# Kernel optimization log

Hardware: AMD Instinct MI355X
Metric: run time of the kernel (lower is better)

Reference implementation:

```python
import jax, jax.numpy as jnp
import numpy as np

N = 100000        # nodes
E_HALF = 800000   # random edges before symmetrization
HID = 128         # hidden_dim
K = 4             # Chebyshev order
NEG = 0.01        # leaky_relu negative slope
BN_EPS = 1e-5
L2_EPS = 1e-12


def setup_inputs() -> dict:
    key = jax.random.key(0)
    ks = jax.random.split(key, 4)
    x = jax.random.normal(ks[0], (N, 3), dtype=jnp.float32)
    e = jax.random.randint(ks[1], (2, E_HALF), 0, N, dtype=jnp.int32)
    # symmetrize so the sym-normalized Laplacian is well defined
    edge_index = jnp.concatenate([e, e[::-1]], axis=1).astype(jnp.int64)

    def wcheb(k, fin, fout):
        return jax.random.normal(k, (K, fin, fout), dtype=jnp.float32) * np.float32(1.0 / np.sqrt(fin * K))

    wk = jax.random.split(ks[2], 5)
    return {
        "x": x, "edge_index": edge_index,
        "W1": wcheb(wk[0], 3, HID),   "b1": jnp.zeros((HID,), jnp.float32),
        "W2": wcheb(wk[1], HID, HID), "b2": jnp.zeros((HID,), jnp.float32),
        "W3": wcheb(wk[2], HID, HID), "b3": jnp.zeros((HID,), jnp.float32),
        "W4": wcheb(wk[3], HID, HID), "b4": jnp.zeros((HID,), jnp.float32),
        "g1": jnp.ones((HID,), jnp.float32), "be1": jnp.zeros((HID,), jnp.float32),
        "g2": jnp.ones((HID,), jnp.float32), "be2": jnp.zeros((HID,), jnp.float32),
        "g3": jnp.ones((HID,), jnp.float32), "be3": jnp.zeros((HID,), jnp.float32),
        "Wrep": jax.random.normal(wk[4], (HID, 3), dtype=jnp.float32) * np.float32(1.0 / np.sqrt(HID)),
        "brep": jnp.zeros((3,), jnp.float32),
    }


def _cheb(x, src, dst, norm, W, b):
    """PyG ChebConv (sym norm, lambda_max=2): out = sum_k T_k(L_hat) x @ W_k + b."""
    def prop(t):  # (L_hat t)_i = sum_{e: src->dst==i} norm_e * t[src_e]
        return jax.ops.segment_sum(t[src] * norm[:, None], dst, num_segments=N)
    Tx0 = x
    out = Tx0 @ W[0]
    Tx1 = prop(Tx0)
    out = out + Tx1 @ W[1]
    for k in range(2, W.shape[0]):
        Tx2 = 2.0 * prop(Tx1) - Tx0
        out = out + Tx2 @ W[k]
        Tx0, Tx1 = Tx1, Tx2
    return out + b


def _bn(x, g, b):  # BatchNorm1d, training mode (batch stats, biased var)
    mu = x.mean(axis=0)
    var = ((x - mu) ** 2).mean(axis=0)
    return (x - mu) * jax.lax.rsqrt(var + BN_EPS) * g + b


def _leaky(x):
    return jnp.where(x >= 0, x, NEG * x)


def reference(x, edge_index, W1, b1, W2, b2, W3, b3, W4, b4,
              g1, be1, g2, be2, g3, be3, Wrep, brep):
    src, dst = edge_index[0], edge_index[1]
    deg = jax.ops.segment_sum(jnp.ones(src.shape, jnp.float32), src, num_segments=N)
    dinv = jnp.where(deg > 0, jax.lax.rsqrt(jnp.maximum(deg, 1.0)), 0.0)
    # scaled Laplacian L_hat = -D^{-1/2} A D^{-1/2} (zero diagonal) for lambda_max=2
    norm = -(dinv[src] * dinv[dst])  # [E]

    h = _cheb(x.astype(jnp.float32), src, dst, norm, W1, b1)
    h = _bn(_leaky(h), g1, be1)
    h = _cheb(h, src, dst, norm, W2, b2)
    h = _bn(_leaky(h), g2, be2)
    h = _cheb(h, src, dst, norm, W3, b3)
    h = _bn(jnp.maximum(h, 0.0), g3, be3)
    h = _cheb(h, src, dst, norm, W4, b4)
    h = h / jnp.maximum(jnp.linalg.norm(h, axis=1, keepdims=True), L2_EPS)
    return h @ Wrep + brep  # [N, 3]
```

## Files before the change

kernel.cpp:

```cpp
#include <hip/hip_runtime.h>
#include <hip/hip_bf16.h>


#define HID 128
#define NEG 0.01f
#define BN_EPS 1e-5f
#define L2_EPS 1e-12f
#define CAP 64

typedef __attribute__((ext_vector_type(8))) short short8;
typedef __attribute__((ext_vector_type(4))) float floatx4;

__device__ __forceinline__ short f2bf(float f) {
    unsigned u = __float_as_uint(f);
    return (short)((u + 0x7fffu + ((u >> 16) & 1u)) >> 16);
}
__device__ __forceinline__ unsigned pack2bf(float x, float y) {
    return (unsigned)(unsigned short)f2bf(x) | ((unsigned)(unsigned short)f2bf(y) << 16);
}
__device__ __forceinline__ float bflo(unsigned u) { return __uint_as_float(u << 16); }
__device__ __forceinline__ float bfhi(unsigned u) { return __uint_as_float(u & 0xffff0000u); }
__device__ __forceinline__ float bf2f(unsigned short h) { return __uint_as_float((unsigned)h << 16); }

__device__ __forceinline__ float actf(float v, int act) {
    if (act == 0) return v >= 0.f ? v : NEG * v;
    if (act == 1) return v > 0.f ? v : 0.f;
    return v;
}


__global__ __launch_bounds__(256) void k_zero(int* __restrict__ arr, float* __restrict__ S,
                                              const float* __restrict__ x, float* __restrict__ xp, int N) {
    int i = blockIdx.x * 256 + threadIdx.x;
    if (i < N) {
        arr[(size_t)i * CAP] = 0;
        float4 v;
        v.x = x[(size_t)i * 3 + 0];
        v.y = x[(size_t)i * 3 + 1];
        v.z = x[(size_t)i * 3 + 2];
        v.w = 0.f;
        *(float4*)(xp + (size_t)i * 4) = v;
    }
    if (blockIdx.x == 0) {
        for (int k = threadIdx.x; k < 1024; k += 256) S[k] = 0.f;
    }
}

__global__ __launch_bounds__(256) void k_fillpad(const int* __restrict__ src, const int* __restrict__ dst,
                                                 int* __restrict__ arr, int E) {
    int e = blockIdx.x * 256 + threadIdx.x;
    if (e >= E) return;
    int d = dst[e];
    int pos = atomicAdd(&arr[(size_t)d * CAP], 1);
    if (pos < CAP - 1) arr[(size_t)d * CAP + 1 + pos] = src[e];
}

__global__ __launch_bounds__(256) void k_dinv(const int* __restrict__ arr, float* __restrict__ dinv,
                                              int* __restrict__ cnt, int N) {
    int i = blockIdx.x * 256 + threadIdx.x;
    if (i < N) {
        int d = arr[(size_t)i * CAP];
        dinv[i] = d > 0 ? rsqrtf((float)d) : 0.f;
        cnt[i] = d < CAP - 1 ? d : CAP - 1;
    }
}

__global__ __launch_bounds__(256) void k_norm(const int* __restrict__ arr, const int* __restrict__ cnt,
                                              const float* __restrict__ dinv, int2* __restrict__ edges,
                                              float* __restrict__ snorm, int N) {
    int node = blockIdx.x * 4 + (threadIdx.x >> 6);
    if (node >= N) return;
    node = __builtin_amdgcn_readfirstlane(node);
    int lane = threadIdx.x & 63;
    int deg = cnt[node];
    float dd = dinv[node];
    int s = (lane < deg) ? arr[(size_t)node * CAP + 1 + lane] : 0;
    float w = (lane < deg) ? -(dinv[s] * dd) : 0.f;
    if (lane < deg) {
        int2 rec;
        rec.x = s;
        rec.y = __float_as_int(w);
        edges[(size_t)node * CAP + lane] = rec;
    }
    float sw = w;
    #pragma unroll
    for (int d = 1; d < 64; d <<= 1) sw += __shfl_xor(sw, d);
    if (lane == 0) snorm[node] = sw;
}


__global__ __launch_bounds__(256) void k_prop3(const float* __restrict__ T, const float* __restrict__ prev,
                                               float* __restrict__ out, const int* __restrict__ cnt,
                                               const int2* __restrict__ edges,
                                               float a, float b, int N) {
    int i = blockIdx.x * 256 + threadIdx.x;
    if (i >= N) return;
    int deg = cnt[i];
    const int2* eb = edges + (size_t)i * CAP;
    float a0 = 0.f, a1 = 0.f, a2 = 0.f;
    int j = 0;
    for (; j + 4 <= deg; j += 4) {
        int2 r0 = eb[j + 0], r1 = eb[j + 1], r2 = eb[j + 2], r3 = eb[j + 3];
        float4 v0 = *(const float4*)(T + (size_t)r0.x * 4);
        float4 v1 = *(const float4*)(T + (size_t)r1.x * 4);
        float4 v2 = *(const float4*)(T + (size_t)r2.x * 4);
        float4 v3 = *(const float4*)(T + (size_t)r3.x * 4);
        float w0 = __int_as_float(r0.y), w1 = __int_as_float(r1.y);
        float w2 = __int_as_float(r2.y), w3 = __int_as_float(r3.y);
        a0 += w0 * v0.x + w1 * v1.x + w2 * v2.x + w3 * v3.x;
        a1 += w0 * v0.y + w1 * v1.y + w2 * v2.y + w3 * v3.y;
        a2 += w0 * v0.z + w1 * v1.z + w2 * v2.z + w3 * v3.z;
    }
    for (; j < deg; ++j) {
        int2 r = eb[j];
        float w = __int_as_float(r.y);
        float4 v = *(const float4*)(T + (size_t)r.x * 4);
        a0 += w * v.x;
        a1 += w * v.y;
        a2 += w * v.z;
    }
    float r0 = a * a0, r1 = a * a1, r2 = a * a2;
    if (prev) {
        const float* pp = prev + (size_t)i * 4;
        r0 += b * pp[0];
        r1 += b * pp[1];
        r2 += b * pp[2];
    }
    float4 o;
    o.x = r0; o.y = r1; o.z = r2; o.w = 0.f;
    *(float4*)(out + (size_t)i * 4) = o;
}

__global__ __launch_bounds__(256) void k_prop1(const unsigned* __restrict__ OUT,
                                               unsigned* __restrict__ T1, unsigned* __restrict__ T0,
                                               const int* __restrict__ cnt, const int2* __restrict__ edges,
                                               const float* __restrict__ snorm, const float* __restrict__ S,
                                               const float* __restrict__ g, const float* __restrict__ be,
                                               int act, float invN, int N) {
    int node = blockIdx.x * 4 + (threadIdx.x >> 6);
    if (node >= N) return;
    node = __builtin_amdgcn_readfirstlane(node);
    int lane = threadIdx.x & 63;
    int f0 = 2 * lane;
    float mu0 = S[f0] * invN, mu1 = S[f0 + 1] * invN;
    float v0 = S[f0 + 128] * invN - mu0 * mu0;
    float v1 = S[f0 + 129] * invN - mu1 * mu1;
    float a0 = g[f0] * rsqrtf(v0 + BN_EPS), a1 = g[f0 + 1] * rsqrtf(v1 + BN_EPS);
    float c0 = be[f0] - mu0 * a0, c1 = be[f0 + 1] - mu1 * a1;

    int deg = cnt[node];
    const int2* eb = edges + (size_t)node * CAP;
    float accx = 0.f, accy = 0.f;
    int j = 0;
    int nb = deg >> 3;
    if (nb > 0) {
        int2 recA[8]; unsigned tA[8];
        int2 recB[8]; unsigned tB[8];
        #pragma unroll
        for (int k = 0; k < 8; ++k) recA[k] = eb[k];
        #pragma unroll
        for (int k = 0; k < 8; ++k) tA[k] = OUT[(size_t)recA[k].x * 64 + lane];
        for (int bi = 1; bi < nb; ++bi) {
            const int2* ebb = eb + bi * 8;
            #pragma unroll
            for (int k = 0; k < 8; ++k) recB[k] = ebb[k];
            #pragma unroll
            for (int k = 0; k < 8; ++k) tB[k] = OUT[(size_t)recB[k].x * 64 + lane];
            #pragma unroll
            for (int k = 0; k < 8; ++k) {
                float w = __int_as_float(recA[k].y);
                accx += w * actf(bflo(tA[k]), act);
                accy += w * actf(bfhi(tA[k]), act);
            }
            #pragma unroll
            for (int k = 0; k < 8; ++k) { recA[k] = recB[k]; tA[k] = tB[k]; }
        }
        #pragma unroll
        for (int k = 0; k < 8; ++k) {
            float w = __int_as_float(recA[k].y);
            accx += w * actf(bflo(tA[k]), act);
            accy += w * actf(bfhi(tA[k]), act);
        }
        j = nb * 8;
    }
    for (; j < deg; ++j) {
        int2 r = eb[j];
        float w = __int_as_float(r.y);
        unsigned t0 = OUT[(size_t)r.x * 64 + lane];
        accx += w * actf(bflo(t0), act);
        accy += w * actf(bfhi(t0), act);
    }
    float si = snorm[node];
    __builtin_nontemporal_store(pack2bf(a0 * accx + si * c0, a1 * accy + si * c1),
                                &T1[(size_t)node * 64 + lane]);
    unsigned h = OUT[(size_t)node * 64 + lane];
    float t0lo = a0 * actf(bflo(h), act) + c0;
    float t0hi = a1 * actf(bfhi(h), act) + c1;
    __builtin_nontemporal_store(pack2bf(t0lo, t0hi), &T0[(size_t)node * 64 + lane]);
}

__global__ __launch_bounds__(256) void k_prop128(const unsigned* __restrict__ T, const unsigned* __restrict__ prev,
                                                 unsigned* __restrict__ out, const int* __restrict__ cnt,
                                                 const int2* __restrict__ edges,
                                                 float a, float b, int N) {
    int node = blockIdx.x * 4 + (threadIdx.x >> 6);
    if (node >= N) return;
    node = __builtin_amdgcn_readfirstlane(node);
    int lane = threadIdx.x & 63;
    int deg = cnt[node];
    const int2* eb = edges + (size_t)node * CAP;
    float accx = 0.f, accy = 0.f;
    int j = 0;
    int nb = deg >> 3;
    if (nb > 0) {
        int2 recA[8]; unsigned tA[8];
        int2 recB[8]; unsigned tB[8];
        #pragma unroll
        for (int k = 0; k < 8; ++k) recA[k] = eb[k];
        #pragma unroll
        for (int k = 0; k < 8; ++k) tA[k] = T[(size_t)recA[k].x * 64 + lane];
        for (int bi = 1; bi < nb; ++bi) {
            const int2* ebb = eb + bi * 8;
            #pragma unroll
            for (int k = 0; k < 8; ++k) recB[k] = ebb[k];
            #pragma unroll
            for (int k = 0; k < 8; ++k) tB[k] = T[(size_t)recB[k].x * 64 + lane];
            #pragma unroll
            for (int k = 0; k < 8; ++k) {
                float w = __int_as_float(recA[k].y);
                accx += w * bflo(tA[k]);
                accy += w * bfhi(tA[k]);
            }
            #pragma unroll
            for (int k = 0; k < 8; ++k) { recA[k] = recB[k]; tA[k] = tB[k]; }
        }
        #pragma unroll
        for (int k = 0; k < 8; ++k) {
            float w = __int_as_float(recA[k].y);
            accx += w * bflo(tA[k]);
            accy += w * bfhi(tA[k]);
        }
        j = nb * 8;
    }
    for (; j < deg; ++j) {
        int2 r = eb[j];
        float w = __int_as_float(r.y);
        unsigned t0 = T[(size_t)r.x * 64 + lane];
        accx += w * bflo(t0);
        accy += w * bfhi(t0);
    }
    float rx = a * accx, ry = a * accy;
    if (prev) {
        unsigned p = __builtin_nontemporal_load(&prev[(size_t)node * 64 + lane]);
        rx += b * bflo(p);
        ry += b * bfhi(p);
    }
    __builtin_nontemporal_store(pack2bf(rx, ry), &out[(size_t)node * 64 + lane]);
}


__global__ __launch_bounds__(256) void k_gemm1(const float* __restrict__ x, const float* __restrict__ t1,
                                               const float* __restrict__ t2, const float* __restrict__ t3,
                                               const float* __restrict__ W, const float* __restrict__ b,
                                               unsigned short* __restrict__ OUT, float* __restrict__ S,
                                               int npb, int N) {
    __shared__ float Wl[12 * 128];
    __shared__ float bl[128];
    __shared__ float sS[256];
    int tid = threadIdx.x;
    for (int i = tid; i < 1536; i += 256) Wl[i] = W[i];
    if (tid < 128) bl[tid] = b[tid];
    if (tid < 256) sS[tid] = 0.f;
    __syncthreads();
    int f = tid & 127;
    int base = blockIdx.x * npb;
    int end = base + npb < N ? base + npb : N;
    const float* rows[4] = {x, t1, t2, t3};
    float s1 = 0.f, s2 = 0.f;
    for (int node = base + (tid >> 7); node < end; node += 2) {
        float acc = bl[f];
        #pragma unroll
        for (int k = 0; k < 4; ++k) {
            float4 rv = *(const float4*)(rows[k] + (size_t)node * 4);
            acc += rv.x * Wl[(k * 3 + 0) * 128 + f];
            acc += rv.y * Wl[(k * 3 + 1) * 128 + f];
            acc += rv.z * Wl[(k * 3 + 2) * 128 + f];
        }
        unsigned short h = (unsigned short)f2bf(acc);
        OUT[(size_t)node * 128 + f] = h;
        float u = actf(bf2f(h), 0);
        s1 += u;
        s2 += u * u;
    }
    atomicAdd(&sS[f], s1);
    atomicAdd(&sS[f + 128], s2);
    __syncthreads();
    if (tid < 256) atomicAdd(&S[tid], sS[tid]);
}


__global__ __launch_bounds__(256) void k_packW(const float* __restrict__ WA, const float* __restrict__ WB,
                                               const float* __restrict__ WC, short* __restrict__ Wp) {
    int gid = blockIdx.x * 256 + threadIdx.x;
    int L = gid >> 16;
    int idx = gid & 65535;
    int j = idx & 7;
    int lane = (idx >> 3) & 63;
    int rest = idx >> 9;
    int nt = rest & 7;
    int ks = rest >> 3;
    int kk = ks * 32 + (lane >> 4) * 8 + j;
    int c = nt * 16 + (lane & 15);
    const float* W = (L == 0) ? WA : (L == 1) ? WB : WC;
    Wp[gid] = f2bf(W[(size_t)(kk >> 7) * 16384 + (kk & 127) * 128 + c]);
}

__global__ __launch_bounds__(512) void k_gemm512(const short* __restrict__ T0, const short* __restrict__ T1,
                                                 const short* __restrict__ T2, const short* __restrict__ T3,
                                                 const short* __restrict__ Wp, const float* __restrict__ bias,
                                                 unsigned short* __restrict__ OUT, float* __restrict__ S,
                                                 const float* __restrict__ Wrep, const float* __restrict__ brep,
                                                 float* __restrict__ fout,
                                                 int M, int doStats, int doFinal, int act) {
    __shared__ short Wlds[65536];
    __shared__ float sS[256];
    __shared__ float sW[388];
    int tid = threadIdx.x;
    int lane = tid & 63, wave = tid >> 6;
    if (tid < 256) sS[tid] = 0.f;
    if (doFinal) {
        for (int i = tid; i < 384; i += 512) sW[i] = Wrep[i];
        if (tid < 3) sW[384 + tid] = brep[tid];
    }
    for (int i = tid; i < 8192; i += 512) ((int4*)Wlds)[i] = ((const int4*)Wp)[i];
    __syncthreads();

    int quad = lane >> 4;
    int col0 = lane & 15;
    const short* Ts[4] = {T0, T1, T2, T3};
    float s1[8], s2[8];
    #pragma unroll
    for (int i = 0; i < 8; ++i) { s1[i] = 0.f; s2[i] = 0.f; }

    int nt32 = (M + 31) / 32;
    int stride = gridDim.x * 8;
    for (int t = blockIdx.x * 8 + wave; t < nt32; t += stride) {
        int r0 = t * 32;
        int rowa = r0 + col0;
        int rowb = rowa + 16;
        size_t rb0 = (size_t)(rowa < M ? rowa : M - 1) * 128;
        size_t rb1 = (size_t)(rowb < M ? rowb : M - 1) * 128;
        floatx4 acc0[8], acc1[8];
        #pragma unroll
        for (int i = 0; i < 8; ++i) {
            acc0[i][0] = 0.f; acc0[i][1] = 0.f; acc0[i][2] = 0.f; acc0[i][3] = 0.f;
            acc1[i][0] = 0.f; acc1[i][1] = 0.f; acc1[i][2] = 0.f; acc1[i][3] = 0.f;
        }
        #pragma unroll 4
        for (int ks = 0; ks < 16; ++ks) {
            const short* Tm = Ts[ks >> 2];
            int aoff = (ks & 3) * 32 + quad * 8;
            short8 af0 = *((const short8*)(Tm + rb0 + aoff));
            short8 af1 = *((const short8*)(Tm + rb1 + aoff));
            #pragma unroll
            for (int nt = 0; nt < 8; ++nt) {
                short8 bf = *((const short8*)(Wlds + ((ks * 8 + nt) * 64 + lane) * 8));
                acc0[nt] = __builtin_amdgcn_mfma_f32_16x16x32_bf16(af0, bf, acc0[nt], 0, 0, 0);
                acc1[nt] = __builtin_amdgcn_mfma_f32_16x16x32_bf16(af1, bf, acc1[nt], 0, 0, 0);
            }
        }
        if (doFinal) {
            #pragma unroll
            for (int half = 0; half < 2; ++half) {
                #pragma unroll
                for (int rg = 0; rg < 4; ++rg) {
                    int r = r0 + half * 16 + quad * 4 + rg;
                    float sq = 0.f, p0 = 0.f, p1 = 0.f, p2 = 0.f;
                    #pragma unroll
                    for (int nt = 0; nt < 8; ++nt) {
                        int c = nt * 16 + col0;
                        float v = (half ? acc1[nt][rg] : acc0[nt][rg]) + bias[c];
                        sq += v * v;
                        p0 += v * sW[c * 3 + 0];
                        p1 += v * sW[c * 3 + 1];
                        p2 += v * sW[c * 3 + 2];
                    }
                    #pragma unroll
                    for (int d = 1; d < 16; d <<= 1) {
                        sq += __shfl_xor(sq, d);
                        p0 += __shfl_xor(p0, d);
                        p1 += __shfl_xor(p1, d);
                        p2 += __shfl_xor(p2, d);
                    }
                    if (col0 == 0 && r < M) {
                        float inv = 1.f / fmaxf(sqrtf(sq), L2_EPS);
                        fout[r * 3 + 0] = p0 * inv + sW[384];
                        fout[r * 3 + 1] = p1 * inv + sW[385];
                        fout[r * 3 + 2] = p2 * inv + sW[386];
                    }
                }
            }
        } else {
            #pragma unroll
            for (int half = 0; half < 2; ++half) {
                int rbase = r0 + half * 16 + quad * 4;
                #pragma unroll
                for (int nt = 0; nt < 8; ++nt) {
                    int c = nt * 16 + col0;
                    float bv = bias[c];
                    #pragma unroll
                    for (int rg = 0; rg < 4; ++rg) {
                        int r = rbase + rg;
                        if (r < M) {
                            float v = (half ? acc1[nt][rg] : acc0[nt][rg]) + bv;
                            unsigned short h = (unsigned short)f2bf(v);
                            OUT[(size_t)r * 128 + c] = h;
                            float u = actf(bf2f(h), act);
                            s1[nt] += u;
                            s2[nt] += u * u;
                        }
                    }
                }
            }
        }
    }
    if (doStats) {
        #pragma unroll
        for (int nt = 0; nt < 8; ++nt) {
            int c = nt * 16 + col0;
            atomicAdd(&sS[c], s1[nt]);
            atomicAdd(&sS[c + 128], s2[nt]);
        }
        __syncthreads();
        if (tid < 256) atomicAdd(&S[tid], sS[tid]);
    }
}


extern "C" void kernel_launch(void* const* d_in, const int* in_sizes, int n_in,
                              void* d_out, int out_size, void* d_ws, size_t ws_size,
                              hipStream_t stream) {
    const int N = in_sizes[0] / 3;
    const int E = in_sizes[1] / 2;

    const float* x    = (const float*)d_in[0];
    const int*   ei   = (const int*)d_in[1];
    const int* esrc = ei;
    const int* edst = ei + E;
    const float* W1 = (const float*)d_in[2];  const float* b1 = (const float*)d_in[3];
    const float* W2 = (const float*)d_in[4];  const float* b2 = (const float*)d_in[5];
    const float* W3 = (const float*)d_in[6];  const float* b3 = (const float*)d_in[7];
    const float* W4 = (const float*)d_in[8];  const float* b4 = (const float*)d_in[9];
    const float* g1 = (const float*)d_in[10]; const float* be1 = (const float*)d_in[11];
    const float* g2 = (const float*)d_in[12]; const float* be2 = (const float*)d_in[13];
    const float* g3 = (const float*)d_in[14]; const float* be3 = (const float*)d_in[15];
    const float* Wrep = (const float*)d_in[16]; const float* brep = (const float*)d_in[17];
    float* out = (float*)d_out;

    char* w = (char*)d_ws;
    size_t off = 0;
    auto alloc = [&](size_t bytes) { size_t o = off; off = (off + bytes + 255) & ~(size_t)255; return o; };
    int*   arr    = (int*)(w + alloc((size_t)N * CAP * 4));
    int*   cnt    = (int*)(w + alloc((size_t)N * 4));
    float* dinv   = (float*)(w + alloc((size_t)N * 4));
    float* snorm  = (float*)(w + alloc((size_t)N * 4));
    int2*  edges  = (int2*)(w + alloc((size_t)N * CAP * 8));
    short* Wp     = (short*)(w + alloc(3 * 65536 * 2));
    float* S      = (float*)(w + alloc(4 * 256 * 4));
    float* xp     = (float*)(w + alloc((size_t)N * 4 * 4));
    float* t1f    = (float*)(w + alloc((size_t)N * 4 * 4));
    float* t2f    = (float*)(w + alloc((size_t)N * 4 * 4));
    float* t3f    = (float*)(w + alloc((size_t)N * 4 * 4));
    short* T0     = (short*)(w + alloc((size_t)N * 128 * 2));
    short* T1     = (short*)(w + alloc((size_t)N * 128 * 2));
    short* T2     = (short*)(w + alloc((size_t)N * 128 * 2));
    short* T3     = (short*)(w + alloc((size_t)N * 128 * 2));
    unsigned short* OUT = (unsigned short*)(w + alloc((size_t)N * 128 * 2));

    int gE = (E + 255) / 256;
    int gN = (N + 255) / 256;
    int gW = (N + 3) / 4;
    float invN = 1.f / (float)N;
    int npb = (N + 255) / 256;

    k_zero<<<gN, 256, 0, stream>>>(arr, S, x, xp, N);
    k_fillpad<<<gE, 256, 0, stream>>>(esrc, edst, arr, E);
    k_dinv<<<gN, 256, 0, stream>>>(arr, dinv, cnt, N);
    k_norm<<<gW, 256, 0, stream>>>(arr, cnt, dinv, edges, snorm, N);
    k_packW<<<768, 256, 0, stream>>>(W2, W3, W4, Wp);

    k_prop3<<<gN, 256, 0, stream>>>(xp, nullptr, t1f, cnt, edges, 1.f, 0.f, N);
    k_prop3<<<gN, 256, 0, stream>>>(t1f, xp, t2f, cnt, edges, 2.f, -1.f, N);
    k_prop3<<<gN, 256, 0, stream>>>(t2f, t1f, t3f, cnt, edges, 2.f, -1.f, N);
    k_gemm1<<<256, 256, 0, stream>>>(xp, t1f, t2f, t3f, W1, b1, OUT, S, npb, N);

    const float* bs[3]  = {b2, b3, b4};
    const float* gs[3]  = {g2, g3, nullptr};
    const float* bes[3] = {be2, be3, nullptr};
    int actsIn[3] = {0, 0, 1};
    int actsOut[3] = {0, 1, 2};

    for (int l = 0; l < 3; ++l) {
        float* Sin = S + (size_t)l * 256;
        float* Sout = S + (size_t)(l + 1) * 256;
        const float* gc = (l == 0) ? g1 : gs[l - 1];
        const float* bc = (l == 0) ? be1 : bes[l - 1];
        k_prop1<<<gW, 256, 0, stream>>>((const unsigned*)OUT, (unsigned*)T1, (unsigned*)T0,
                                        cnt, edges, snorm, Sin, gc, bc, actsIn[l], invN, N);
        k_prop128<<<gW, 256, 0, stream>>>((const unsigned*)T1, (const unsigned*)T0, (unsigned*)T2,
                                          cnt, edges, 2.f, -1.f, N);
        k_prop128<<<gW, 256, 0, stream>>>((const unsigned*)T2, (const unsigned*)T1, (unsigned*)T3,
                                          cnt, edges, 2.f, -1.f, N);
        k_gemm512<<<256, 512, 0, stream>>>(T0, T1, T2, T3, Wp + (size_t)l * 65536, bs[l], OUT, Sout,
                                           Wrep, brep, out, N,
                                           l < 2 ? 1 : 0, l == 2 ? 1 : 0, actsOut[l]);
    }
}
```

Measured before the change: 1.065 ms.

## Split wavefront into two half-waves gathering 8-byte rows with zero-padded edge lists

The 128-feature propagation kernels now split each wavefront into two 32-lane halves. Each half gathers whole bf16 rows with 8-byte loads from alternating edges, and the halves are combined with a cross-half shuffle. k_norm pads each node's edge list with zero-weight records up to a multiple of 16, so the scalar tail loop is removed and every gather runs in fixed 16-edge blocks. This aims to issue fewer, wider memory requests and more independent gathers per wave. In exchange, padded zero-weight edges still cost loads, and only half the lanes do the final store.

```diff
diff --git a/kernel.cpp b/kernel.cpp
--- a/kernel.cpp
+++ b/kernel.cpp
@@ -10,6 +10,7 @@
 
 typedef __attribute__((ext_vector_type(8))) short short8;
 typedef __attribute__((ext_vector_type(4))) float floatx4;
+typedef __attribute__((ext_vector_type(2))) unsigned uintx2;
 
 __device__ __forceinline__ short f2bf(float f) {
     unsigned u = __float_as_uint(f);
@@ -73,10 +74,11 @@
     node = __builtin_amdgcn_readfirstlane(node);
     int lane = threadIdx.x & 63;
     int deg = cnt[node];
+    int degp = (deg + 15) & ~15;
     float dd = dinv[node];
     int s = (lane < deg) ? arr[(size_t)node * CAP + 1 + lane] : 0;
     float w = (lane < deg) ? -(dinv[s] * dd) : 0.f;
-    if (lane < deg) {
+    if (lane < degp) {
         int2 rec;
         rec.x = s;
         rec.y = __float_as_int(w);
@@ -141,36 +143,48 @@
     if (node >= N) return;
     node = __builtin_amdgcn_readfirstlane(node);
     int lane = threadIdx.x & 63;
-    int f0 = 2 * lane;
-    float mu0 = S[f0] * invN, mu1 = S[f0 + 1] * invN;
-    float v0 = S[f0 + 128] * invN - mu0 * mu0;
-    float v1 = S[f0 + 129] * invN - mu1 * mu1;
-    float a0 = g[f0] * rsqrtf(v0 + BN_EPS), a1 = g[f0 + 1] * rsqrtf(v1 + BN_EPS);
-    float c0 = be[f0] - mu0 * a0, c1 = be[f0 + 1] - mu1 * a1;
+    int half = lane >> 5;
+    int m = lane & 31;
+    float4 sv1 = *(const float4*)(S + 4 * m);
+    float4 sv2 = *(const float4*)(S + 128 + 4 * m);
+    float4 gv  = *(const float4*)(g + 4 * m);
+    float4 bev = *(const float4*)(be + 4 * m);
+    float A0, A1, A2, A3, C0, C1, C2, C3;
+    {
+        float mu0 = sv1.x * invN, mu1 = sv1.y * invN, mu2 = sv1.z * invN, mu3 = sv1.w * invN;
+        A0 = gv.x * rsqrtf(sv2.x * invN - mu0 * mu0 + BN_EPS);
+        A1 = gv.y * rsqrtf(sv2.y * invN - mu1 * mu1 + BN_EPS);
+        A2 = gv.z * rsqrtf(sv2.z * invN - mu2 * mu2 + BN_EPS);
+        A3 = gv.w * rsqrtf(sv2.w * invN - mu3 * mu3 + BN_EPS);
+        C0 = bev.x - mu0 * A0; C1 = bev.y - mu1 * A1;
+        C2 = bev.z - mu2 * A2; C3 = bev.w - mu3 * A3;
+    }
 
     int deg = cnt[node];
+    int degp = (deg + 15) & ~15;
     const int2* eb = edges + (size_t)node * CAP;
-    float accx = 0.f, accy = 0.f;
-    int j = 0;
-    int nb = deg >> 3;
+    float ax = 0.f, ay = 0.f, az = 0.f, aw = 0.f;
+    int nb = degp >> 4;
     if (nb > 0) {
-        int2 recA[8]; unsigned tA[8];
-        int2 recB[8]; unsigned tB[8];
-        #pragma unroll
-        for (int k = 0; k < 8; ++k) recA[k] = eb[k];
-        #pragma unroll
-        for (int k = 0; k < 8; ++k) tA[k] = OUT[(size_t)recA[k].x * 64 + lane];
+        int2 recA[8]; uintx2 tA[8];
+        int2 recB[8]; uintx2 tB[8];
+        #pragma unroll
+        for (int k = 0; k < 8; ++k) recA[k] = eb[2 * k + half];
+        #pragma unroll
+        for (int k = 0; k < 8; ++k) tA[k] = *(const uintx2*)(OUT + (size_t)recA[k].x * 64 + m * 2);
         for (int bi = 1; bi < nb; ++bi) {
-            const int2* ebb = eb + bi * 8;
-            #pragma unroll
-            for (int k = 0; k < 8; ++k) recB[k] = ebb[k];
-            #pragma unroll
-            for (int k = 0; k < 8; ++k) tB[k] = OUT[(size_t)recB[k].x * 64 + lane];
+            const int2* ebb = eb + bi * 16;
+            #pragma unroll
+            for (int k = 0; k < 8; ++k) recB[k] = ebb[2 * k + half];
+            #pragma unroll
+            for (int k = 0; k < 8; ++k) tB[k] = *(const uintx2*)(OUT + (size_t)recB[k].x * 64 + m * 2);
             #pragma unroll
             for (int k = 0; k < 8; ++k) {
                 float w = __int_as_float(recA[k].y);
-                accx += w * actf(bflo(tA[k]), act);
-                accy += w * actf(bfhi(tA[k]), act);
+                ax += w * actf(bflo(tA[k].x), act);
+                ay += w * actf(bfhi(tA[k].x), act);
+                az += w * actf(bflo(tA[k].y), act);
+                aw += w * actf(bfhi(tA[k].y), act);
             }
             #pragma unroll
             for (int k = 0; k < 8; ++k) { recA[k] = recB[k]; tA[k] = tB[k]; }
@@ -178,25 +192,26 @@
         #pragma unroll
         for (int k = 0; k < 8; ++k) {
             float w = __int_as_float(recA[k].y);
-            accx += w * actf(bflo(tA[k]), act);
-            accy += w * actf(bfhi(tA[k]), act);
-        }
-        j = nb * 8;
-    }
-    for (; j < deg; ++j) {
-        int2 r = eb[j];
-        float w = __int_as_float(r.y);
-        unsigned t0 = OUT[(size_t)r.x * 64 + lane];
-        accx += w * actf(bflo(t0), act);
-        accy += w * actf(bfhi(t0), act);
-    }
-    float si = snorm[node];
-    __builtin_nontemporal_store(pack2bf(a0 * accx + si * c0, a1 * accy + si * c1),
-                                &T1[(size_t)node * 64 + lane]);
-    unsigned h = OUT[(size_t)node * 64 + lane];
-    float t0lo = a0 * actf(bflo(h), act) + c0;
-    float t0hi = a1 * actf(bfhi(h), act) + c1;
-    __builtin_nontemporal_store(pack2bf(t0lo, t0hi), &T0[(size_t)node * 64 + lane]);
+            ax += w * actf(bflo(tA[k].x), act);
+            ay += w * actf(bfhi(tA[k].x), act);
+            az += w * actf(bflo(tA[k].y), act);
+            aw += w * actf(bfhi(tA[k].y), act);
+        }
+    }
+    ax += __shfl_xor(ax, 32); ay += __shfl_xor(ay, 32);
+    az += __shfl_xor(az, 32); aw += __shfl_xor(aw, 32);
+    if (half == 0) {
+        float si = snorm[node];
+        uintx2 o;
+        o.x = pack2bf(A0 * ax + si * C0, A1 * ay + si * C1);
+        o.y = pack2bf(A2 * az + si * C2, A3 * aw + si * C3);
+        __builtin_nontemporal_store(o, (uintx2*)T1 + (size_t)node * 32 + m);
+        uintx2 h = *((const uintx2*)OUT + (size_t)node * 32 + m);
+        uintx2 t;
+        t.x = pack2bf(A0 * actf(bflo(h.x), act) + C0, A1 * actf(bfhi(h.x), act) + C1);
+        t.y = pack2bf(A2 * actf(bflo(h.y), act) + C2, A3 * actf(bfhi(h.y), act) + C3);
+        __builtin_nontemporal_store(t, (uintx2*)T0 + (size_t)node * 32 + m);
+    }
 }
 
 __global__ __launch_bounds__(256) void k_prop128(const unsigned* __restrict__ T, const unsigned* __restrict__ prev,
@@ -207,29 +222,33 @@
     if (node >= N) return;
     node = __builtin_amdgcn_readfirstlane(node);
     int lane = threadIdx.x & 63;
+    int half = lane >> 5;
+    int m = lane & 31;
     int deg = cnt[node];
+    int degp = (deg + 15) & ~15;
     const int2* eb = edges + (size_t)node * CAP;
-    float accx = 0.f, accy = 0.f;
-    int j = 0;
-    int nb = deg >> 3;
+    float ax = 0.f, ay = 0.f, az = 0.f, aw = 0.f;
+    int nb = degp >> 4;
     if (nb > 0) {
-        int2 recA[8]; unsigned tA[8];
-        int2 recB[8]; unsigned tB[8];
-        #pragma unroll
-        for (int k = 0; k < 8; ++k) recA[k] = eb[k];
-        #pragma unroll
-        for (int k = 0; k < 8; ++k) tA[k] = T[(size_t)recA[k].x * 64 + lane];
+        int2 recA[8]; uintx2 tA[8];
+        int2 recB[8]; uintx2 tB[8];
+        #pragma unroll
+        for (int k = 0; k < 8; ++k) recA[k] = eb[2 * k + half];
+        #pragma unroll
+        for (int k = 0; k < 8; ++k) tA[k] = *(const uintx2*)(T + (size_t)recA[k].x * 64 + m * 2);
         for (int bi = 1; bi < nb; ++bi) {
-            const int2* ebb = eb + bi * 8;
-            #pragma unroll
-            for (int k = 0; k < 8; ++k) recB[k] = ebb[k];
-            #pragma unroll
-            for (int k = 0; k < 8; ++k) tB[k] = T[(size_t)recB[k].x * 64 + lane];
+            const int2* ebb = eb + bi * 16;
+            #pragma unroll
+            for (int k = 0; k < 8; ++k) recB[k] = ebb[2 * k + half];
+            #pragma unroll
+            for (int k = 0; k < 8; ++k) tB[k] = *(const uintx2*)(T + (size_t)recB[k].x * 64 + m * 2);
             #pragma unroll
             for (int k = 0; k < 8; ++k) {
                 float w = __int_as_float(recA[k].y);
-                accx += w * bflo(tA[k]);
-                accy += w * bfhi(tA[k]);
+                ax += w * bflo(tA[k].x);
+                ay += w * bfhi(tA[k].x);
+                az += w * bflo(tA[k].y);
+                aw += w * bfhi(tA[k].y);
             }
             #pragma unroll
             for (int k = 0; k < 8; ++k) { recA[k] = recB[k]; tA[k] = tB[k]; }
@@ -237,25 +256,26 @@
         #pragma unroll
         for (int k = 0; k < 8; ++k) {
             float w = __int_as_float(recA[k].y);
-            accx += w * bflo(tA[k]);
-            accy += w * bfhi(tA[k]);
-        }
-        j = nb * 8;
-    }
-    for (; j < deg; ++j) {
-        int2 r = eb[j];
-        float w = __int_as_float(r.y);
-        unsigned t0 = T[(size_t)r.x * 64 + lane];
-        accx += w * bflo(t0);
-        accy += w * bfhi(t0);
-    }
-    float rx = a * accx, ry = a * accy;
-    if (prev) {
-        unsigned p = __builtin_nontemporal_load(&prev[(size_t)node * 64 + lane]);
-        rx += b * bflo(p);
-        ry += b * bfhi(p);
-    }
-    __builtin_nontemporal_store(pack2bf(rx, ry), &out[(size_t)node * 64 + lane]);
+            ax += w * bflo(tA[k].x);
+            ay += w * bfhi(tA[k].x);
+            az += w * bflo(tA[k].y);
+            aw += w * bfhi(tA[k].y);
+        }
+    }
+    ax += __shfl_xor(ax, 32); ay += __shfl_xor(ay, 32);
+    az += __shfl_xor(az, 32); aw += __shfl_xor(aw, 32);
+    if (half == 0) {
+        float rx = a * ax, ry = a * ay, rz = a * az, rw = a * aw;
+        if (prev) {
+            uintx2 p = *((const uintx2*)prev + (size_t)node * 32 + m);
+            rx += b * bflo(p.x); ry += b * bfhi(p.x);
+            rz += b * bflo(p.y); rw += b * bfhi(p.y);
+        }
+        uintx2 o;
+        o.x = pack2bf(rx, ry);
+        o.y = pack2bf(rz, rw);
+        __builtin_nontemporal_store(o, (uintx2*)out + (size_t)node * 32 + m);
+    }
 }
 
 
```

Measured after the change: 1.289 ms. +21.1%, slower.
